# Kernel tuning notes

Measured on AMD Instinct MI355X. Metric: run time of the kernel, lower is better.

Reference implementation:

```python
import jax, jax.numpy as jnp
import numpy as np

N_HEADS = 16
SCALE = 8.0  # sqrt(inner_dim // n_heads) = sqrt(64), scale='inv_sqrt'


def setup_inputs() -> dict:
    key = jax.random.key(0)
    k1, k2, k3, k4 = jax.random.split(key, 4)
    b, n, d_model, inner = 8, 2048, 1024, 1024
    x = jax.random.normal(k1, (b, n, d_model), dtype=jnp.float32)
    Wqkv = jax.random.normal(k2, (3 * inner, d_model), dtype=jnp.float32) * (1.0 / np.sqrt(d_model))
    Wproj = jax.random.normal(k3, (d_model, inner), dtype=jnp.float32) * (1.0 / np.sqrt(inner))
    bproj = jax.random.normal(k4, (d_model,), dtype=jnp.float32) * 0.01
    return {"x": x, "Wqkv": Wqkv, "Wproj": Wproj, "bproj": bproj}


def reference(x, Wqkv, Wproj, bproj):
    b, n, _ = x.shape
    qkv = jnp.einsum('bnm,fm->bnf', x, Wqkv)          # [b, n, 3*inner]
    qkv = qkv.reshape(b, n, N_HEADS, -1)              # [b, n, h, 3*dh] (einops 'b n (h d)')
    dh = qkv.shape[3] // 3
    q, k, v = qkv[..., :dh], qkv[..., dh:2 * dh], qkv[..., 2 * dh:]
    # Faithful to source: q @ k.transpose(-1,-2) on [b,n,h,dh] -> scores over HEADS, [b,n,h,h]
    scores = jnp.einsum('bnhd,bngd->bnhg', q, k) / SCALE
    attn = jax.nn.softmax(scores, axis=-1)            # softmax over last head axis
    out = jnp.einsum('bnhg,bngd->bnhd', attn, v)      # [b, n, h, dh]
    out = out.reshape(b, n, -1)                       # [b, n, inner]
    return jnp.einsum('bni,mi->bnm', out, Wproj) + bproj
```

## Files before the change

kernel.cpp:

```cpp
#include <hip/hip_runtime.h>
#include <stdint.h>

typedef __bf16 bf16_t;
typedef __bf16 bf16x8 __attribute__((ext_vector_type(8)));
typedef float f32x4 __attribute__((ext_vector_type(4)));

__device__ __forceinline__ void gload_lds16(const void* g, void* l) {
  __builtin_amdgcn_global_load_lds(
      (const __attribute__((address_space(1))) uint32_t*)g,
      (__attribute__((address_space(3))) uint32_t*)l, 16, 0, 0);
}

__global__ void cast3_f32_bf16(const float* __restrict__ a, bf16_t* __restrict__ ao, int n4a,
                               const float* __restrict__ b, bf16_t* __restrict__ bo, int n4b,
                               const float* __restrict__ c, bf16_t* __restrict__ co, int n4c) {
  int i = blockIdx.x * blockDim.x + threadIdx.x;
  int stride = gridDim.x * blockDim.x;
  int total = n4a + n4b + n4c;
  for (int idx = i; idx < total; idx += stride) {
    const float* src; bf16_t* dst; int j = idx;
    if (j < n4a) { src = a; dst = ao; }
    else if ((j -= n4a) < n4b) { src = b; dst = bo; }
    else { j -= n4b; src = c; dst = co; }
    float4 v = reinterpret_cast<const float4*>(src)[j];
    union { bf16_t b[4]; uint2 u; } pk;
    pk.b[0] = (bf16_t)v.x; pk.b[1] = (bf16_t)v.y;
    pk.b[2] = (bf16_t)v.z; pk.b[3] = (bf16_t)v.w;
    reinterpret_cast<uint2*>(dst)[j] = pk.u;
  }
}

template <bool BF16_OUT>
__global__ __launch_bounds__(512, 2)
void gemm_pipe(const bf16_t* __restrict__ A, const bf16_t* __restrict__ B,
               void* __restrict__ Cout, const float* __restrict__ bias,
               int N) {
  constexpr int K = 1024, NT = 32;
  __shared__ bf16_t Al[4][256 * 32];
  __shared__ bf16_t Bl[4][256 * 32];

  const int tid = threadIdx.x;
  const int l = tid & 63, w = tid >> 6;
  const int wm = w >> 2, wn = w & 3;

  const int bid = blockIdx.x;
  const int xcd = bid & 7;
  const int idx = bid >> 3;
  const int bx = xcd * 8 + (idx & 7);
  const int by = idx >> 3;
  const int m0 = bx * 256, n0 = by * 256;

  const int ra = tid >> 2;
  const int ca = ((tid & 3) ^ ((tid >> 3) & 3)) * 8;
  const bf16_t* pA0 = A + (size_t)(m0 +   0 + ra) * K + ca;
  const bf16_t* pA1 = A + (size_t)(m0 + 128 + ra) * K + ca;
  const bf16_t* pB0 = B + (size_t)(n0 +   0 + ra) * K + ca;
  const bf16_t* pB1 = B + (size_t)(n0 + 128 + ra) * K + ca;
  const int wb = w * 512;

#define STAGE_A(t_, s_) do { const int kt_ = (t_) * 32;          \
    gload_lds16(pA0 + kt_, &Al[s_][wb]);                         \
    gload_lds16(pA1 + kt_, &Al[s_][4096 + wb]); } while (0)
#define STAGE_B(t_, s_) do { const int kt_ = (t_) * 32;          \
    gload_lds16(pB0 + kt_, &Bl[s_][wb]);                         \
    gload_lds16(pB1 + kt_, &Bl[s_][4096 + wb]); } while (0)

  const int abase = (wm * 128 + (l & 15)) * 32;
  const int bbase = (wn * 64 + (l & 15)) * 32;
  const int ck = ((l >> 4) ^ ((l >> 1) & 3)) * 8;

  f32x4 acc[8][4] = {};

  STAGE_A(0, 0); STAGE_B(0, 0);
  STAGE_A(1, 1); STAGE_B(1, 1);
  STAGE_A(2, 2); STAGE_B(2, 2);
  asm volatile("s_waitcnt vmcnt(8)" ::: "memory");
  __builtin_amdgcn_s_barrier();

  for (int t = 0; t < NT; ++t) {
    const int slot = t & 3;
    const int s3 = (t + 3) & 3;
    const bf16_t* As = Al[slot];
    const bf16_t* Bs = Bl[slot];
    bf16x8 af0[4], af1[4], bfr[4];

#pragma unroll
    for (int i = 0; i < 4; ++i)
      af0[i] = *reinterpret_cast<const bf16x8*>(&As[abase + i * 512 + ck]);
#pragma unroll
    for (int j = 0; j < 4; ++j)
      bfr[j] = *reinterpret_cast<const bf16x8*>(&Bs[bbase + j * 512 + ck]);
    if (t + 3 < NT) STAGE_A(t + 3, s3);
    __builtin_amdgcn_s_barrier();
    asm volatile("s_waitcnt lgkmcnt(0)" ::: "memory");
    __builtin_amdgcn_sched_barrier(0);
    __builtin_amdgcn_s_setprio(1);
#pragma unroll
    for (int i = 0; i < 4; ++i)
#pragma unroll
      for (int j = 0; j < 4; ++j)
        acc[i][j] = __builtin_amdgcn_mfma_f32_16x16x32_bf16(af0[i], bfr[j],
                                                            acc[i][j], 0, 0, 0);
    __builtin_amdgcn_s_setprio(0);
    __builtin_amdgcn_s_barrier();

#pragma unroll
    for (int i = 0; i < 4; ++i)
      af1[i] = *reinterpret_cast<const bf16x8*>(&As[abase + (i + 4) * 512 + ck]);
    if (t + 3 < NT) STAGE_B(t + 3, s3);
    __builtin_amdgcn_s_barrier();
    asm volatile("s_waitcnt lgkmcnt(0)" ::: "memory");
    __builtin_amdgcn_sched_barrier(0);
    __builtin_amdgcn_s_setprio(1);
#pragma unroll
    for (int i = 0; i < 4; ++i)
#pragma unroll
      for (int j = 0; j < 4; ++j)
        acc[i + 4][j] = __builtin_amdgcn_mfma_f32_16x16x32_bf16(af1[i], bfr[j],
                                                                acc[i + 4][j], 0, 0, 0);
    __builtin_amdgcn_s_setprio(0);
    if (t + 3 < NT)       asm volatile("s_waitcnt vmcnt(8)" ::: "memory");
    else if (t == NT - 3) asm volatile("s_waitcnt vmcnt(4)" ::: "memory");
    else if (t == NT - 2) asm volatile("s_waitcnt vmcnt(0)" ::: "memory");
    __builtin_amdgcn_s_barrier();
  }
#undef STAGE_A
#undef STAGE_B

  const int r0 = m0 + wm * 128 + (l >> 4) * 4;
  const int c0 = n0 + wn * 64 + (l & 15);
  if (BF16_OUT) {
    bf16_t* C = (bf16_t*)Cout;
#pragma unroll
    for (int i = 0; i < 8; ++i)
#pragma unroll
      for (int j = 0; j < 4; ++j)
#pragma unroll
        for (int r = 0; r < 4; ++r)
          C[(size_t)(r0 + i * 16 + r) * N + (c0 + j * 16)] = (bf16_t)acc[i][j][r];
  } else {
    float* C = (float*)Cout;
#pragma unroll
    for (int i = 0; i < 8; ++i)
#pragma unroll
      for (int j = 0; j < 4; ++j)
#pragma unroll
        for (int r = 0; r < 4; ++r)
          C[(size_t)(r0 + i * 16 + r) * N + (c0 + j * 16)] =
              acc[i][j][r] + bias[c0 + j * 16];
  }
}

__global__ __launch_bounds__(256)
void attn_heads(const bf16_t* __restrict__ qkv, bf16_t* __restrict__ out) {
  __shared__ float s[4][3072];
  const int w = threadIdx.x >> 6, l = threadIdx.x & 63;
  const size_t t = (size_t)blockIdx.x * 4 + w;
  const bf16_t* src = qkv + t * 3072;
#pragma unroll
  for (int i = 0; i < 6; ++i) {
    int f = (i * 64 + l) * 8;
    bf16x8 v = *reinterpret_cast<const bf16x8*>(&src[f]);
#pragma unroll
    for (int jj = 0; jj < 8; ++jj) s[w][f + jj] = (float)v[jj];
  }
  __syncthreads();

  const int h = l >> 2, ss = l & 3;
  float qr[16];
  const float* qb = &s[w][h * 192 + ss * 16];
#pragma unroll
  for (int d = 0; d < 16; ++d) qr[d] = qb[d];

  float sc[16];
#pragma unroll
  for (int g = 0; g < 16; ++g) {
    const float* kk = &s[w][g * 192 + 64 + ss * 16];
    float p = 0.f;
#pragma unroll
    for (int d = 0; d < 16; ++d) p += qr[d] * kk[d];
    p += __shfl_xor(p, 1);
    p += __shfl_xor(p, 2);
    sc[g] = p * 0.125f;
  }
  float m = sc[0];
#pragma unroll
  for (int g = 1; g < 16; ++g) m = fmaxf(m, sc[g]);
  float sum = 0.f;
#pragma unroll
  for (int g = 0; g < 16; ++g) { sc[g] = __expf(sc[g] - m); sum += sc[g]; }
  float inv = 1.f / sum;

  float o[16] = {};
#pragma unroll
  for (int g = 0; g < 16; ++g) {
    float a = sc[g] * inv;
    const float* vv = &s[w][g * 192 + 128 + ss * 16];
#pragma unroll
    for (int d = 0; d < 16; ++d) o[d] += a * vv[d];
  }
  union { bf16_t b[16]; uint4 u[2]; } pk;
#pragma unroll
  for (int d = 0; d < 16; ++d) pk.b[d] = (bf16_t)o[d];
  uint4* dst = reinterpret_cast<uint4*>(out + t * 1024 + h * 64 + ss * 16);
  dst[0] = pk.u[0];
  dst[1] = pk.u[1];
}

extern "C" void kernel_launch(void* const* d_in, const int* in_sizes, int n_in,
                              void* d_out, int out_size, void* d_ws, size_t ws_size,
                              hipStream_t stream) {
  const float* x     = (const float*)d_in[0];
  const float* Wqkv  = (const float*)d_in[1];
  const float* Wproj = (const float*)d_in[2];
  const float* bproj = (const float*)d_in[3];
  float* out = (float*)d_out;

  const int M = 8 * 2048;
  const int DM = 1024;
  const int F = 3072;

  char* ws = (char*)d_ws;
  bf16_t* xb     = (bf16_t*)ws;  ws += (size_t)M * DM * 2;
  bf16_t* wqkvb  = (bf16_t*)ws;  ws += (size_t)F * DM * 2;
  bf16_t* wprojb = (bf16_t*)ws;  ws += (size_t)DM * DM * 2;
  bf16_t* qkvb   = (bf16_t*)ws;  ws += (size_t)M * F * 2;
  bf16_t* attnb  = (bf16_t*)ws;

  cast3_f32_bf16<<<2048, 256, 0, stream>>>(x, xb, M * DM / 4,
                                           Wqkv, wqkvb, F * DM / 4,
                                           Wproj, wprojb, DM * DM / 4);

  gemm_pipe<true><<<(M / 256) * (F / 256), 512, 0, stream>>>(
      xb, wqkvb, (void*)qkvb, nullptr, F);

  attn_heads<<<M / 4, 256, 0, stream>>>(qkvb, attnb);

  gemm_pipe<false><<<(M / 256) * (DM / 256), 512, 0, stream>>>(
      attnb, wprojb, (void*)out, bproj, DM);
}
```

Baseline: 214.9 us.

## Shrink GEMM block tile to 256x128 with 4 waves and 3-stage LDS ring

The GEMM block tile changes from 256x256 with 8 waves to 256x128 with 4 waves, each wave still computing 128x64. The LDS pipeline drops from 4 stages to 3 (prefetch distance 2), with the loads split differently between the two half-iterations and the vmcnt waits adjusted to match. Together this cuts LDS use per block (about 72KB instead of 128KB), doubles the grid size, and aims for more blocks resident per CU and better load balance. The costs are lower reuse of the B tile, more global traffic for A, and a shorter prefetch distance that hides less latency.

```diff
diff --git a/kernel.cpp b/kernel.cpp
--- a/kernel.cpp
+++ b/kernel.cpp
@@ -31,39 +31,43 @@
 }
 
 template <bool BF16_OUT>
-__global__ __launch_bounds__(512, 2)
+__global__ __launch_bounds__(256, 2)
 void gemm_pipe(const bf16_t* __restrict__ A, const bf16_t* __restrict__ B,
                void* __restrict__ Cout, const float* __restrict__ bias,
                int N) {
   constexpr int K = 1024, NT = 32;
-  __shared__ bf16_t Al[4][256 * 32];
-  __shared__ bf16_t Bl[4][256 * 32];
+  __shared__ bf16_t Al[3][256 * 32];
+  __shared__ bf16_t Bl[3][128 * 32];
 
   const int tid = threadIdx.x;
   const int l = tid & 63, w = tid >> 6;
-  const int wm = w >> 2, wn = w & 3;
+  const int wm = w >> 1, wn = w & 1;
 
   const int bid = blockIdx.x;
   const int xcd = bid & 7;
   const int idx = bid >> 3;
   const int bx = xcd * 8 + (idx & 7);
   const int by = idx >> 3;
-  const int m0 = bx * 256, n0 = by * 256;
+  const int m0 = bx * 256, n0 = by * 128;
 
   const int ra = tid >> 2;
   const int ca = ((tid & 3) ^ ((tid >> 3) & 3)) * 8;
   const bf16_t* pA0 = A + (size_t)(m0 +   0 + ra) * K + ca;
-  const bf16_t* pA1 = A + (size_t)(m0 + 128 + ra) * K + ca;
+  const bf16_t* pA1 = A + (size_t)(m0 +  64 + ra) * K + ca;
+  const bf16_t* pA2 = A + (size_t)(m0 + 128 + ra) * K + ca;
+  const bf16_t* pA3 = A + (size_t)(m0 + 192 + ra) * K + ca;
   const bf16_t* pB0 = B + (size_t)(n0 +   0 + ra) * K + ca;
-  const bf16_t* pB1 = B + (size_t)(n0 + 128 + ra) * K + ca;
-  const int wb = w * 512;
-
-#define STAGE_A(t_, s_) do { const int kt_ = (t_) * 32;          \
-    gload_lds16(pA0 + kt_, &Al[s_][wb]);                         \
-    gload_lds16(pA1 + kt_, &Al[s_][4096 + wb]); } while (0)
-#define STAGE_B(t_, s_) do { const int kt_ = (t_) * 32;          \
-    gload_lds16(pB0 + kt_, &Bl[s_][wb]);                         \
-    gload_lds16(pB1 + kt_, &Bl[s_][4096 + wb]); } while (0)
+  const bf16_t* pB1 = B + (size_t)(n0 +  64 + ra) * K + ca;
+  const int wb = tid * 8;
+
+#define STAGE_P0(t_, s_) do { const int kt_ = (t_) * 32;         \
+    gload_lds16(pA0 + kt_, &Al[s_][0 * 2048 + wb]);              \
+    gload_lds16(pA1 + kt_, &Al[s_][1 * 2048 + wb]);              \
+    gload_lds16(pA2 + kt_, &Al[s_][2 * 2048 + wb]); } while (0)
+#define STAGE_P1(t_, s_) do { const int kt_ = (t_) * 32;         \
+    gload_lds16(pA3 + kt_, &Al[s_][3 * 2048 + wb]);              \
+    gload_lds16(pB0 + kt_, &Bl[s_][0 * 2048 + wb]);              \
+    gload_lds16(pB1 + kt_, &Bl[s_][1 * 2048 + wb]); } while (0)
 
   const int abase = (wm * 128 + (l & 15)) * 32;
   const int bbase = (wn * 64 + (l & 15)) * 32;
@@ -71,15 +75,14 @@
 
   f32x4 acc[8][4] = {};
 
-  STAGE_A(0, 0); STAGE_B(0, 0);
-  STAGE_A(1, 1); STAGE_B(1, 1);
-  STAGE_A(2, 2); STAGE_B(2, 2);
-  asm volatile("s_waitcnt vmcnt(8)" ::: "memory");
+  STAGE_P0(0, 0); STAGE_P1(0, 0);
+  STAGE_P0(1, 1); STAGE_P1(1, 1);
+  asm volatile("s_waitcnt vmcnt(6)" ::: "memory");
   __builtin_amdgcn_s_barrier();
 
+  int slot = 0;
   for (int t = 0; t < NT; ++t) {
-    const int slot = t & 3;
-    const int s3 = (t + 3) & 3;
+    int s2 = slot + 2; if (s2 >= 3) s2 -= 3;
     const bf16_t* As = Al[slot];
     const bf16_t* Bs = Bl[slot];
     bf16x8 af0[4], af1[4], bfr[4];
@@ -90,7 +93,7 @@
 #pragma unroll
     for (int j = 0; j < 4; ++j)
       bfr[j] = *reinterpret_cast<const bf16x8*>(&Bs[bbase + j * 512 + ck]);
-    if (t + 3 < NT) STAGE_A(t + 3, s3);
+    if (t + 2 < NT) STAGE_P0(t + 2, s2);
     __builtin_amdgcn_s_barrier();
     asm volatile("s_waitcnt lgkmcnt(0)" ::: "memory");
     __builtin_amdgcn_sched_barrier(0);
@@ -107,7 +110,7 @@
 #pragma unroll
     for (int i = 0; i < 4; ++i)
       af1[i] = *reinterpret_cast<const bf16x8*>(&As[abase + (i + 4) * 512 + ck]);
-    if (t + 3 < NT) STAGE_B(t + 3, s3);
+    if (t + 2 < NT) STAGE_P1(t + 2, s2);
     __builtin_amdgcn_s_barrier();
     asm volatile("s_waitcnt lgkmcnt(0)" ::: "memory");
     __builtin_amdgcn_sched_barrier(0);
@@ -119,13 +122,13 @@
         acc[i + 4][j] = __builtin_amdgcn_mfma_f32_16x16x32_bf16(af1[i], bfr[j],
                                                                 acc[i + 4][j], 0, 0, 0);
     __builtin_amdgcn_s_setprio(0);
-    if (t + 3 < NT)       asm volatile("s_waitcnt vmcnt(8)" ::: "memory");
-    else if (t == NT - 3) asm volatile("s_waitcnt vmcnt(4)" ::: "memory");
+    if (t + 2 < NT)       asm volatile("s_waitcnt vmcnt(6)" ::: "memory");
     else if (t == NT - 2) asm volatile("s_waitcnt vmcnt(0)" ::: "memory");
     __builtin_amdgcn_s_barrier();
-  }
-#undef STAGE_A
-#undef STAGE_B
+    slot = (slot == 2) ? 0 : slot + 1;
+  }
+#undef STAGE_P0
+#undef STAGE_P1
 
   const int r0 = m0 + wm * 128 + (l >> 4) * 4;
   const int c0 = n0 + wn * 64 + (l & 15);
@@ -231,11 +234,11 @@
                                            Wqkv, wqkvb, F * DM / 4,
                                            Wproj, wprojb, DM * DM / 4);
 
-  gemm_pipe<true><<<(M / 256) * (F / 256), 512, 0, stream>>>(
+  gemm_pipe<true><<<(M / 256) * (F / 128), 256, 0, stream>>>(
       xb, wqkvb, (void*)qkvb, nullptr, F);
 
   attn_heads<<<M / 4, 256, 0, stream>>>(qkvb, attnb);
 
-  gemm_pipe<false><<<(M / 256) * (DM / 256), 512, 0, stream>>>(
+  gemm_pipe<false><<<(M / 256) * (DM / 128), 256, 0, stream>>>(
       attnb, wprojb, (void*)out, bproj, DM);
 }
```

New measurement: 216.1 us. Within noise of the previous version (+0.6%).
